# Kernel tuning notes

Hardware: AMD Instinct MI355X
Metric: run time of the kernel (lower is better)

Reference implementation:

```python
import jax, jax.numpy as jnp
import numpy as np

N_HEADS = 32
N_KV = 8
HEAD_DIM = 128
EPS = 1e-5

def _rope(t, fr, fi):
    # t: [b,s,h,hd] -> pairs [b,s,h,hd/2,2]; fr/fi: [s,hd/2]
    tp = t.astype(jnp.float32).reshape(*t.shape[:-1], HEAD_DIM // 2, 2)
    a, b = tp[..., 0], tp[..., 1]
    fr = fr[None, :, None, :]
    fi = fi[None, :, None, :]
    out = jnp.stack([a * fr - b * fi, a * fi + b * fr], axis=-1)
    return out.reshape(t.shape).astype(t.dtype)

def _rmsnorm(t):
    tf = t.astype(jnp.float32)
    return (tf * jax.lax.rsqrt(jnp.mean(tf * tf, axis=-1, keepdims=True) + EPS)).astype(t.dtype)

def setup_inputs() -> dict:
    key = jax.random.key(0)
    ks = jax.random.split(key, 5)
    b, s, dim = 1, 2048, 4096
    x = jax.random.normal(ks[0], (b, s, dim), dtype=jnp.float32) * 0.02
    wq = jax.random.normal(ks[1], (dim, dim), dtype=jnp.float32) * 0.02
    wk = jax.random.normal(ks[2], (N_KV * HEAD_DIM, dim), dtype=jnp.float32) * 0.02
    wv = jax.random.normal(ks[3], (N_KV * HEAD_DIM, dim), dtype=jnp.float32) * 0.02
    wo = jax.random.normal(ks[4], (dim, dim), dtype=jnp.float32) * 0.02
    # RoPE freqs, llama-style theta=10000
    inv = 1.0 / (10000.0 ** (np.arange(0, HEAD_DIM, 2, dtype=np.float32) / HEAD_DIM))
    ang = np.outer(np.arange(s, dtype=np.float32), inv)  # [s, hd/2]
    freqs_cis = jnp.asarray(np.stack([np.cos(ang), np.sin(ang)], axis=-1))  # [s, hd/2, 2]
    # causal additive mask
    mask = jnp.where(jnp.tril(jnp.ones((s, s), dtype=bool)), 0.0, -1e30).astype(jnp.float32)
    return {"x": x, "wq": wq, "wk": wk, "wv": wv, "wo": wo,
            "freqs_cis": freqs_cis, "mask": mask, "start_pos": 0}

def reference(x, wq, wk, wv, wo, freqs_cis, mask, start_pos):
    b, s, dim = x.shape
    n_rep = N_HEADS // N_KV
    xq = jnp.einsum('bsd,ed->bse', x, wq).reshape(b, s, N_HEADS, HEAD_DIM)
    xk = jnp.einsum('bsd,ed->bse', x, wk).reshape(b, s, N_KV, HEAD_DIM)
    xv = jnp.einsum('bsd,ed->bse', x, wv).reshape(b, s, N_KV, HEAD_DIM)
    fr, fi = freqs_cis[..., 0], freqs_cis[..., 1]
    xq = _rope(xq, fr, fi)
    xk = _rope(xk, fr, fi)
    xq = _rmsnorm(xq)
    xk = _rmsnorm(xk)
    # start_pos=0 prefill: KV cache write/read is identity on xk/xv
    q = xq.transpose(0, 2, 1, 3).reshape(b, N_KV, n_rep, s, HEAD_DIM)  # grouped query heads
    k = xk.transpose(0, 2, 1, 3)  # [b, n_kv, s, hd]
    v = xv.transpose(0, 2, 1, 3)
    scores = jnp.einsum('bkrsd,bktd->bkrst', q, k) / np.sqrt(HEAD_DIM)
    scores = scores + mask[None, None, None, :, :]
    probs = jax.nn.softmax(scores, axis=-1)
    o = jnp.einsum('bkrst,bktd->bkrsd', probs, v)
    o = o.reshape(b, N_HEADS, s, HEAD_DIM).transpose(0, 2, 1, 3).reshape(b, s, dim)
    return jnp.einsum('bse,de->bsd', o, wo)
```

## Files before the change

### kernel.cpp

```cpp
#include <hip/hip_runtime.h>
#include <hip/hip_bf16.h>
#include <cstdint>
#include <cstddef>

using u16 = unsigned short;
using u32 = unsigned int;

typedef __attribute__((ext_vector_type(8))) __bf16 bf16x8;
typedef __attribute__((ext_vector_type(4))) float f32x4;
typedef __attribute__((ext_vector_type(2))) float f32x2;
typedef __attribute__((ext_vector_type(4))) u32 u32x4;

typedef const __attribute__((address_space(1))) void* gas_ptr;
typedef __attribute__((address_space(3))) void* las_ptr;

__device__ __forceinline__ void async_cp16(const void* g, void* l) {
  __builtin_amdgcn_global_load_lds((gas_ptr)g, (las_ptr)l, 16, 0, 0);
}

__device__ __forceinline__ float bf2f(u16 u) {
  u32 v = ((u32)u) << 16;
  return __builtin_bit_cast(float, v);
}
__device__ __forceinline__ u16 f2bf(float f) {
  u32 v = __builtin_bit_cast(u32, f);
  u32 r = (v + 0x7fffu + ((v >> 16) & 1u)) >> 16;
  return (u16)r;
}

__device__ __forceinline__ f32x4 mfma16(bf16x8 a, bf16x8 b, f32x4 c) {
  return __builtin_amdgcn_mfma_f32_16x16x32_bf16(a, b, c, 0, 0, 0);
}

__global__ __launch_bounds__(256) void cvt_f32_bf16(const float* __restrict__ in,
                                                    u16* __restrict__ out, int n8) {
  int i = blockIdx.x * blockDim.x + threadIdx.x;
  int stride = gridDim.x * blockDim.x;
  for (; i < n8; i += stride) {
    const float4* p = (const float4*)(in + (size_t)i * 8);
    float4 a = p[0], b = p[1];
    union { u16 us[8]; u32x4 v; } o;
    o.us[0] = f2bf(a.x); o.us[1] = f2bf(a.y); o.us[2] = f2bf(a.z); o.us[3] = f2bf(a.w);
    o.us[4] = f2bf(b.x); o.us[5] = f2bf(b.y); o.us[6] = f2bf(b.z); o.us[7] = f2bf(b.w);
    *(u32x4*)(out + (size_t)i * 8) = o.v;
  }
}

template <bool F32OUT>
__global__ __launch_bounds__(256, 3) void gemm_bt(const u16* __restrict__ A,
                                                  const u16* __restrict__ B,
                                                  void* __restrict__ Cv,
                                                  int M, int N, int K) {
  __shared__ __align__(16) u16 As[128 * 64];
  __shared__ __align__(16) u16 Bs[128 * 64];
  const int tid = threadIdx.x;
  const int wave = tid >> 6, lane = tid & 63;
  const int quad = lane >> 4, c16 = lane & 15;

  const int mb = M >> 7, nb = N >> 7;
  const int per_xcd_n = nb >> 3;
  const int xcd = blockIdx.x & 7, lid = blockIdx.x >> 3;
  const int m_t = lid % mb, n_local = lid / mb;
  const int m0 = m_t * 128, n0 = (xcd * per_xcd_n + n_local) * 128;

  const int wm = (wave & 1) * 64, wn = (wave >> 1) * 64;

  f32x4 acc[4][4] = {};

  const u16* Ab = A + (size_t)m0 * K;
  const u16* Bb = B + (size_t)n0 * K;

  for (int k0 = 0; k0 < K; k0 += 64) {
    __syncthreads();
#pragma unroll
    for (int i = 0; i < 4; ++i) {
      int idx = tid + 256 * i;
      int row = idx >> 3, sg = (idx & 7) ^ (row & 7);
      async_cp16(Ab + (size_t)row * K + k0 + sg * 8, As + (size_t)idx * 8);
    }
#pragma unroll
    for (int i = 0; i < 4; ++i) {
      int idx = tid + 256 * i;
      int row = idx >> 3, sg = (idx & 7) ^ (row & 7);
      async_cp16(Bb + (size_t)row * K + k0 + sg * 8, Bs + (size_t)idx * 8);
    }
    asm volatile("s_waitcnt vmcnt(0)" ::: "memory");
    __syncthreads();

    bf16x8 af[4][2], bfr[4][2];
#pragma unroll
    for (int mt = 0; mt < 4; ++mt) {
      int row = wm + mt * 16 + c16;
#pragma unroll
      for (int c = 0; c < 2; ++c)
        af[mt][c] = *(const bf16x8*)(As + row * 64 + (((c * 4 + quad) ^ (row & 7)) * 8));
    }
#pragma unroll
    for (int nt = 0; nt < 4; ++nt) {
      int row = wn + nt * 16 + c16;
#pragma unroll
      for (int c = 0; c < 2; ++c)
        bfr[nt][c] = *(const bf16x8*)(Bs + row * 64 + (((c * 4 + quad) ^ (row & 7)) * 8));
    }
#pragma unroll
    for (int c = 0; c < 2; ++c)
#pragma unroll
      for (int mt = 0; mt < 4; ++mt)
#pragma unroll
        for (int nt = 0; nt < 4; ++nt)
          acc[mt][nt] = mfma16(af[mt][c], bfr[nt][c], acc[mt][nt]);
  }

#pragma unroll
  for (int mt = 0; mt < 4; ++mt) {
#pragma unroll
    for (int nt = 0; nt < 4; ++nt) {
#pragma unroll
      for (int r = 0; r < 4; ++r) {
        int gm = m0 + wm + mt * 16 + quad * 4 + r;
        int gn = n0 + wn + nt * 16 + c16;
        float v = acc[mt][nt][r];
        if (F32OUT)
          ((float*)Cv)[(size_t)gm * N + gn] = v;
        else
          ((u16*)Cv)[(size_t)gm * N + gn] = f2bf(v);
      }
    }
  }
}

__global__ __launch_bounds__(256) void transpose_v(const u16* __restrict__ in,
                                                   u16* __restrict__ out) {
  __shared__ __align__(16) u16 t[64 * 72];
  const int bs = blockIdx.x * 64;
  const int be = blockIdx.y * 64;
  const int tid = threadIdx.x;
  {
    const int row = tid >> 3, cc = tid & 7;
#pragma unroll
    for (int pp = 0; pp < 2; ++pp) {
      int r = row + 32 * pp;
      u32x4 v = *(const u32x4*)(in + (size_t)(bs + r) * 6144 + 5120 + be + cc * 8);
      *(u32x4*)(&t[r * 72 + ((cc ^ ((r >> 3) & 7)) * 8)]) = v;
    }
  }
  __syncthreads();
  {
    const int c0 = tid >> 3, rc = tid & 7;
#pragma unroll
    for (int pp = 0; pp < 2; ++pp) {
      int c = c0 + 32 * pp;
      union { u16 us[8]; u32x4 v; } o;
#pragma unroll
      for (int j = 0; j < 8; ++j)
        o.us[j] = t[(rc * 8 + j) * 72 + ((((c >> 3) ^ rc) * 8) + (c & 7))];
      *(u32x4*)(out + (size_t)(be + c) * 2048 + bs + rc * 8) = o.v;
    }
  }
}

__global__ __launch_bounds__(256) void rope_rms(const u16* __restrict__ in, int stride,
                                                u16* __restrict__ out,
                                                const float* __restrict__ freqs,
                                                int n_heads) {
  int gw = blockIdx.x * 4 + (threadIdx.x >> 6);
  int lane = threadIdx.x & 63;
  int s = gw / n_heads, h = gw % n_heads;
  u32 ab = *(const u32*)(in + (size_t)s * stride + h * 128 + lane * 2);
  float a = bf2f((u16)(ab & 0xffff));
  float b = bf2f((u16)(ab >> 16));
  f32x2 ff = *(const f32x2*)(freqs + (size_t)s * 128 + lane * 2);
  float ra = a * ff.x - b * ff.y;
  float rb = a * ff.y + b * ff.x;
  float ss = ra * ra + rb * rb;
#pragma unroll
  for (int m = 32; m; m >>= 1) ss += __shfl_xor(ss, m, 64);
  float r = rsqrtf(ss * (1.0f / 128.0f) + 1e-5f);
  u32 pk = (u32)f2bf(ra * r) | ((u32)f2bf(rb * r) << 16);
  *(u32*)(out + ((size_t)h * 2048 + s) * 128 + lane * 2) = pk;
}

#define SEQ 2048
__global__ __launch_bounds__(256) void attn(const u16* __restrict__ Q,
                                            const u16* __restrict__ Kh,
                                            const u16* __restrict__ VT,
                                            u16* __restrict__ O) {
  __shared__ __align__(16) u16 Ks[2][64 * 128];
  __shared__ __align__(16) u16 Vs[2][128 * 64];
  __shared__ __align__(16) u16 Ps[4][32 * 64];
  const int tid = threadIdx.x;
  const int wave = tid >> 6, lane = tid & 63;
  const int quad = lane >> 4, c16 = lane & 15;
  const int bid = blockIdx.x;
  const int hk = bid & 7;
  const int rest = bid >> 3;
  const int hq = rest >> 3;
  const int p = rest & 7;
  const int h = hk * 4 + hq;

  const float sc = 0.12751743f;
  const float B = 16.5f;
  const u16* Kb = Kh + (size_t)hk * SEQ * 128;
  const u16* Vb = VT + (size_t)hk * 128 * SEQ;

  auto stage = [&](int t0, int b) __attribute__((always_inline)) {
#pragma unroll
    for (int i = 0; i < 4; ++i) {
      int idx = tid + 256 * i;
      int row = idx >> 4, sg = (idx & 15) ^ (row & 7);
      async_cp16(Kb + (size_t)(t0 + row) * 128 + sg * 8, &Ks[b][(size_t)idx * 8]);
    }
#pragma unroll
    for (int i = 0; i < 4; ++i) {
      int idx = tid + 256 * i;
      int row = idx >> 3, sg = (idx & 7) ^ (row & 7);
      async_cp16(Vb + (size_t)row * SEQ + t0 + sg * 8, &Vs[b][(size_t)idx * 8]);
    }
  };

#pragma unroll 1
  for (int tile = 0; tile < 2; ++tile) {
    const int qt = tile ? (15 - p) : p;
    const int q0w = qt * 128 + wave * 32;
    const int kend = qt * 128 + 128;

    bf16x8 qfr[2][4];
    const u16* qbase = Q + (size_t)h * SEQ * 128;
#pragma unroll
    for (int g = 0; g < 2; ++g)
#pragma unroll
      for (int c = 0; c < 4; ++c)
        qfr[g][c] =
            *(const bf16x8*)(qbase + (size_t)(q0w + g * 16 + c16) * 128 + c * 32 + quad * 8);

    f32x4 o_acc[2][8] = {};
    float lsum[2][4] = {};

    __syncthreads();
    stage(0, 0);

#pragma unroll 1
    for (int t0 = 0; t0 < kend; t0 += 64) {
      const int cur = (t0 >> 6) & 1;
      asm volatile("s_waitcnt vmcnt(0)" ::: "memory");
      __syncthreads();
      if (t0 + 64 < kend) stage(t0 + 64, cur ^ 1);

      if (t0 < q0w + 32) {
        f32x4 sa[2][4] = {};
#pragma unroll
        for (int ct = 0; ct < 4; ++ct) {
          int t = ct * 16 + c16;
          int tbase = t * 128;
          int tsw = t & 7;
#pragma unroll
          for (int c = 0; c < 4; ++c) {
            bf16x8 kf = *(const bf16x8*)(&Ks[cur][tbase + (((c * 4 + quad) ^ tsw) * 8)]);
            sa[0][ct] = mfma16(qfr[0][c], kf, sa[0][ct]);
            sa[1][ct] = mfma16(qfr[1][c], kf, sa[1][ct]);
          }
        }

        const bool diag = (t0 + 64 > q0w);
        auto soft = [&](bool masked) __attribute__((always_inline)) {
#pragma unroll
          for (int g = 0; g < 2; ++g) {
#pragma unroll
            for (int r = 0; r < 4; ++r) {
              int row = g * 16 + quad * 4 + r;
              int row_q = q0w + row;
              int rbase = row * 64;
              int rsw = row & 7;
#pragma unroll
              for (int ct = 0; ct < 4; ++ct) {
                float s = sa[g][ct][r];
                float arg = fmaf(s, sc, -B);
                if (masked) {
                  int t_idx = t0 + ct * 16 + c16;
                  arg = (t_idx <= row_q) ? arg : -1.0e30f;
                }
                float pe = exp2f(arg);
                lsum[g][r] += pe;
                u32 pb = (__builtin_bit_cast(u32, pe) + 0x8000u) >> 16;
                Ps[wave][rbase + (((ct * 2 + (c16 >> 3)) ^ rsw) * 8) + (c16 & 7)] = (u16)pb;
              }
            }
          }
        };
        if (diag) soft(true); else soft(false);
        asm volatile("s_waitcnt lgkmcnt(0)" ::: "memory");

#pragma unroll
        for (int tc = 0; tc < 2; ++tc) {
          bf16x8 pf[2];
#pragma unroll
          for (int g = 0; g < 2; ++g) {
            int prow = g * 16 + c16;
            pf[g] = *(const bf16x8*)(&Ps[wave][prow * 64 + (((tc * 4 + quad) ^ (prow & 7)) * 8)]);
          }
#pragma unroll
          for (int nt = 0; nt < 8; ++nt) {
            int dl = nt * 16 + c16;
            bf16x8 vf = *(const bf16x8*)(&Vs[cur][dl * 64 + (((tc * 4 + quad) ^ (dl & 7)) * 8)]);
            o_acc[0][nt] = mfma16(pf[0], vf, o_acc[0][nt]);
            o_acc[1][nt] = mfma16(pf[1], vf, o_acc[1][nt]);
          }
        }
      }
    }

#pragma unroll
    for (int g = 0; g < 2; ++g) {
#pragma unroll
      for (int r = 0; r < 4; ++r) {
        float l = lsum[g][r];
#pragma unroll
        for (int m = 1; m < 16; m <<= 1) l += __shfl_xor(l, m, 64);
        float inv = 1.0f / l;
        int s_idx = q0w + g * 16 + quad * 4 + r;
        u16* ob = O + (size_t)s_idx * 4096 + (size_t)h * 128;
#pragma unroll
        for (int nt = 0; nt < 8; ++nt) ob[nt * 16 + c16] = f2bf(o_acc[g][nt][r] * inv);
      }
    }
  }
}

extern "C" void kernel_launch(void* const* d_in, const int* in_sizes, int n_in,
                              void* d_out, int out_size, void* d_ws, size_t ws_size,
                              hipStream_t stream) {
  const float* x  = (const float*)d_in[0];
  const float* wq = (const float*)d_in[1];
  const float* wk = (const float*)d_in[2];
  const float* wv = (const float*)d_in[3];
  const float* wo = (const float*)d_in[4];
  const float* fr = (const float*)d_in[5];
  float* out = (float*)d_out;

  const size_t S = 2048, D = 4096, KV = 1024, NQKV = D + 2 * KV;
  u16* p = (u16*)d_ws;
  u16* xb     = p; p += S * D;
  u16* wqkv   = p; p += NQKV * D;
  u16* qkvraw = p; p += S * NQKV;
  u16* qh     = p; p += S * D;
  u16* khh    = p; p += S * KV;
  u16* vt     = p; p += KV * S;
  u16* wob = wqkv;
  u16* ob  = qkvraw;

  auto cvt_launch = [&](const float* src, u16* dst, size_t n) {
    int n8 = (int)(n / 8);
    int blocks = (n8 + 255) / 256;
    if (blocks > 2048) blocks = 2048;
    cvt_f32_bf16<<<dim3(blocks), dim3(256), 0, stream>>>(src, dst, n8);
  };

  cvt_launch(x, xb, S * D);
  cvt_launch(wq, wqkv, D * D);
  cvt_launch(wk, wqkv + D * D, KV * D);
  cvt_launch(wv, wqkv + (D + KV) * D, KV * D);

  gemm_bt<false><<<dim3((S / 128) * (NQKV / 128)), dim3(256), 0, stream>>>(
      xb, wqkv, (void*)qkvraw, (int)S, (int)NQKV, (int)D);

  cvt_launch(wo, wob, D * D);

  transpose_v<<<dim3(32, 16), dim3(256), 0, stream>>>(qkvraw, vt);
  rope_rms<<<dim3((int)(S * 32 / 4)), dim3(256), 0, stream>>>(qkvraw, (int)NQKV, qh, fr, 32);
  rope_rms<<<dim3((int)(S * 8 / 4)), dim3(256), 0, stream>>>(qkvraw + D, (int)NQKV, khh, fr, 8);

  attn<<<dim3(256), dim3(256), 0, stream>>>(qh, khh, vt, ob);

  gemm_bt<true><<<dim3((S / 128) * (D / 128)), dim3(256), 0, stream>>>(
      ob, wob, (void*)out, (int)S, (int)D, (int)D);
}
```

Measured before the change: 483.3 us.

## Process paired causal query tiles concurrently in 512-thread attention blocks, fuse input conversions

The attention kernel now uses 512 threads per block. Two 4-wave groups handle the light and heavy query tiles of a causal pair at the same time, sharing one K/V staging pass, where before the two tiles ran one after the other. This avoids loading the light tile's K/V range twice and raises waves per CU; the block-to-head mapping changes and s_setprio hints are added around the MFMA loops. The four fp32-to-bf16 conversions of x, wq, wk and wv are merged into one launch to cut launch overhead. The risk is the light-tile group sitting idle at barriers while the heavy tile iterates, plus higher LDS use per block.

```diff
diff --git a/kernel.cpp b/kernel.cpp
--- a/kernel.cpp
+++ b/kernel.cpp
@@ -43,6 +43,33 @@
     o.us[0] = f2bf(a.x); o.us[1] = f2bf(a.y); o.us[2] = f2bf(a.z); o.us[3] = f2bf(a.w);
     o.us[4] = f2bf(b.x); o.us[5] = f2bf(b.y); o.us[6] = f2bf(b.z); o.us[7] = f2bf(b.w);
     *(u32x4*)(out + (size_t)i * 8) = o.v;
+  }
+}
+
+__global__ __launch_bounds__(256) void cvt4(const float* __restrict__ x,
+                                            const float* __restrict__ wq,
+                                            const float* __restrict__ wk,
+                                            const float* __restrict__ wv,
+                                            u16* __restrict__ xb,
+                                            u16* __restrict__ wqkv) {
+  const int B0 = 1048576;
+  const int B1 = B0 + 2097152;
+  const int B2 = B1 + 524288;
+  const int B3 = B2 + 524288;
+  int i = blockIdx.x * blockDim.x + threadIdx.x;
+  int stride = gridDim.x * blockDim.x;
+  for (; i < B3; i += stride) {
+    const float* src; u16* dst; int j;
+    if (i < B0)      { src = x;  dst = xb;                           j = i; }
+    else if (i < B1) { src = wq; dst = wqkv;                         j = i - B0; }
+    else if (i < B2) { src = wk; dst = wqkv + (size_t)4096 * 4096;   j = i - B1; }
+    else             { src = wv; dst = wqkv + (size_t)5120 * 4096;   j = i - B2; }
+    const float4* p = (const float4*)(src + (size_t)j * 8);
+    float4 a = p[0], b = p[1];
+    union { u16 us[8]; u32x4 v; } o;
+    o.us[0] = f2bf(a.x); o.us[1] = f2bf(a.y); o.us[2] = f2bf(a.z); o.us[3] = f2bf(a.w);
+    o.us[4] = f2bf(b.x); o.us[5] = f2bf(b.y); o.us[6] = f2bf(b.z); o.us[7] = f2bf(b.w);
+    *(u32x4*)(dst + (size_t)j * 8) = o.v;
   }
 }
 
@@ -181,22 +208,27 @@
 }
 
 #define SEQ 2048
-__global__ __launch_bounds__(256) void attn(const u16* __restrict__ Q,
-                                            const u16* __restrict__ Kh,
-                                            const u16* __restrict__ VT,
-                                            u16* __restrict__ O) {
+__global__ __launch_bounds__(512, 2) void attn(const u16* __restrict__ Q,
+                                               const u16* __restrict__ Kh,
+                                               const u16* __restrict__ VT,
+                                               u16* __restrict__ O) {
   __shared__ __align__(16) u16 Ks[2][64 * 128];
   __shared__ __align__(16) u16 Vs[2][128 * 64];
-  __shared__ __align__(16) u16 Ps[4][32 * 64];
+  __shared__ __align__(16) u16 Ps[8][32 * 64];
   const int tid = threadIdx.x;
   const int wave = tid >> 6, lane = tid & 63;
   const int quad = lane >> 4, c16 = lane & 15;
   const int bid = blockIdx.x;
   const int hk = bid & 7;
   const int rest = bid >> 3;
-  const int hq = rest >> 3;
-  const int p = rest & 7;
+  const int hq = rest & 3;
+  const int p = rest >> 2;
   const int h = hk * 4 + hq;
+
+  const int wl = wave & 3, grp = wave >> 2;
+  const int qt = grp ? p : (15 - p);
+  const int q0w = qt * 128 + wl * 32;
+  const int kend = (15 - p) * 128 + 128;
 
   const float sc = 0.12751743f;
   const float B = 16.5f;
@@ -205,123 +237,119 @@
 
   auto stage = [&](int t0, int b) __attribute__((always_inline)) {
 #pragma unroll
-    for (int i = 0; i < 4; ++i) {
-      int idx = tid + 256 * i;
+    for (int i = 0; i < 2; ++i) {
+      int idx = tid + 512 * i;
       int row = idx >> 4, sg = (idx & 15) ^ (row & 7);
       async_cp16(Kb + (size_t)(t0 + row) * 128 + sg * 8, &Ks[b][(size_t)idx * 8]);
     }
 #pragma unroll
-    for (int i = 0; i < 4; ++i) {
-      int idx = tid + 256 * i;
+    for (int i = 0; i < 2; ++i) {
+      int idx = tid + 512 * i;
       int row = idx >> 3, sg = (idx & 7) ^ (row & 7);
       async_cp16(Vb + (size_t)row * SEQ + t0 + sg * 8, &Vs[b][(size_t)idx * 8]);
     }
   };
 
+  bf16x8 qfr[2][4];
+  const u16* qbase = Q + (size_t)h * SEQ * 128;
+#pragma unroll
+  for (int g = 0; g < 2; ++g)
+#pragma unroll
+    for (int c = 0; c < 4; ++c)
+      qfr[g][c] =
+          *(const bf16x8*)(qbase + (size_t)(q0w + g * 16 + c16) * 128 + c * 32 + quad * 8);
+
+  f32x4 o_acc[2][8] = {};
+  float lsum[2][4] = {};
+
+  stage(0, 0);
+
 #pragma unroll 1
-  for (int tile = 0; tile < 2; ++tile) {
-    const int qt = tile ? (15 - p) : p;
-    const int q0w = qt * 128 + wave * 32;
-    const int kend = qt * 128 + 128;
-
-    bf16x8 qfr[2][4];
-    const u16* qbase = Q + (size_t)h * SEQ * 128;
-#pragma unroll
-    for (int g = 0; g < 2; ++g)
-#pragma unroll
-      for (int c = 0; c < 4; ++c)
-        qfr[g][c] =
-            *(const bf16x8*)(qbase + (size_t)(q0w + g * 16 + c16) * 128 + c * 32 + quad * 8);
-
-    f32x4 o_acc[2][8] = {};
-    float lsum[2][4] = {};
-
+  for (int t0 = 0; t0 < kend; t0 += 64) {
+    const int cur = (t0 >> 6) & 1;
+    asm volatile("s_waitcnt vmcnt(0)" ::: "memory");
     __syncthreads();
-    stage(0, 0);
-
-#pragma unroll 1
-    for (int t0 = 0; t0 < kend; t0 += 64) {
-      const int cur = (t0 >> 6) & 1;
-      asm volatile("s_waitcnt vmcnt(0)" ::: "memory");
-      __syncthreads();
-      if (t0 + 64 < kend) stage(t0 + 64, cur ^ 1);
-
-      if (t0 < q0w + 32) {
-        f32x4 sa[2][4] = {};
-#pragma unroll
-        for (int ct = 0; ct < 4; ++ct) {
-          int t = ct * 16 + c16;
-          int tbase = t * 128;
-          int tsw = t & 7;
-#pragma unroll
-          for (int c = 0; c < 4; ++c) {
-            bf16x8 kf = *(const bf16x8*)(&Ks[cur][tbase + (((c * 4 + quad) ^ tsw) * 8)]);
-            sa[0][ct] = mfma16(qfr[0][c], kf, sa[0][ct]);
-            sa[1][ct] = mfma16(qfr[1][c], kf, sa[1][ct]);
+    if (t0 + 64 < kend) stage(t0 + 64, cur ^ 1);
+
+    if (t0 < q0w + 32) {
+      f32x4 sa[2][4] = {};
+      __builtin_amdgcn_s_setprio(1);
+#pragma unroll
+      for (int ct = 0; ct < 4; ++ct) {
+        int t = ct * 16 + c16;
+        int tbase = t * 128;
+        int tsw = t & 7;
+#pragma unroll
+        for (int c = 0; c < 4; ++c) {
+          bf16x8 kf = *(const bf16x8*)(&Ks[cur][tbase + (((c * 4 + quad) ^ tsw) * 8)]);
+          sa[0][ct] = mfma16(qfr[0][c], kf, sa[0][ct]);
+          sa[1][ct] = mfma16(qfr[1][c], kf, sa[1][ct]);
+        }
+      }
+      __builtin_amdgcn_s_setprio(0);
+
+      const bool diag = (t0 + 64 > q0w);
+      auto soft = [&](bool masked) __attribute__((always_inline)) {
+#pragma unroll
+        for (int g = 0; g < 2; ++g) {
+#pragma unroll
+          for (int r = 0; r < 4; ++r) {
+            int row = g * 16 + quad * 4 + r;
+            int row_q = q0w + row;
+            int rbase = row * 64;
+            int rsw = row & 7;
+#pragma unroll
+            for (int ct = 0; ct < 4; ++ct) {
+              float s = sa[g][ct][r];
+              float arg = fmaf(s, sc, -B);
+              if (masked) {
+                int t_idx = t0 + ct * 16 + c16;
+                arg = (t_idx <= row_q) ? arg : -1.0e30f;
+              }
+              float pe = exp2f(arg);
+              lsum[g][r] += pe;
+              u32 pb = (__builtin_bit_cast(u32, pe) + 0x8000u) >> 16;
+              Ps[wave][rbase + (((ct * 2 + (c16 >> 3)) ^ rsw) * 8) + (c16 & 7)] = (u16)pb;
+            }
           }
         }
-
-        const bool diag = (t0 + 64 > q0w);
-        auto soft = [&](bool masked) __attribute__((always_inline)) {
-#pragma unroll
-          for (int g = 0; g < 2; ++g) {
-#pragma unroll
-            for (int r = 0; r < 4; ++r) {
-              int row = g * 16 + quad * 4 + r;
-              int row_q = q0w + row;
-              int rbase = row * 64;
-              int rsw = row & 7;
-#pragma unroll
-              for (int ct = 0; ct < 4; ++ct) {
-                float s = sa[g][ct][r];
-                float arg = fmaf(s, sc, -B);
-                if (masked) {
-                  int t_idx = t0 + ct * 16 + c16;
-                  arg = (t_idx <= row_q) ? arg : -1.0e30f;
-                }
-                float pe = exp2f(arg);
-                lsum[g][r] += pe;
-                u32 pb = (__builtin_bit_cast(u32, pe) + 0x8000u) >> 16;
-                Ps[wave][rbase + (((ct * 2 + (c16 >> 3)) ^ rsw) * 8) + (c16 & 7)] = (u16)pb;
-              }
-            }
-          }
-        };
-        if (diag) soft(true); else soft(false);
-        asm volatile("s_waitcnt lgkmcnt(0)" ::: "memory");
-
-#pragma unroll
-        for (int tc = 0; tc < 2; ++tc) {
-          bf16x8 pf[2];
-#pragma unroll
-          for (int g = 0; g < 2; ++g) {
-            int prow = g * 16 + c16;
-            pf[g] = *(const bf16x8*)(&Ps[wave][prow * 64 + (((tc * 4 + quad) ^ (prow & 7)) * 8)]);
-          }
-#pragma unroll
-          for (int nt = 0; nt < 8; ++nt) {
-            int dl = nt * 16 + c16;
-            bf16x8 vf = *(const bf16x8*)(&Vs[cur][dl * 64 + (((tc * 4 + quad) ^ (dl & 7)) * 8)]);
-            o_acc[0][nt] = mfma16(pf[0], vf, o_acc[0][nt]);
-            o_acc[1][nt] = mfma16(pf[1], vf, o_acc[1][nt]);
-          }
+      };
+      if (diag) soft(true); else soft(false);
+      asm volatile("s_waitcnt lgkmcnt(0)" ::: "memory");
+
+      __builtin_amdgcn_s_setprio(1);
+#pragma unroll
+      for (int tc = 0; tc < 2; ++tc) {
+        bf16x8 pf[2];
+#pragma unroll
+        for (int g = 0; g < 2; ++g) {
+          int prow = g * 16 + c16;
+          pf[g] = *(const bf16x8*)(&Ps[wave][prow * 64 + (((tc * 4 + quad) ^ (prow & 7)) * 8)]);
+        }
+#pragma unroll
+        for (int nt = 0; nt < 8; ++nt) {
+          int dl = nt * 16 + c16;
+          bf16x8 vf = *(const bf16x8*)(&Vs[cur][dl * 64 + (((tc * 4 + quad) ^ (dl & 7)) * 8)]);
+          o_acc[0][nt] = mfma16(pf[0], vf, o_acc[0][nt]);
+          o_acc[1][nt] = mfma16(pf[1], vf, o_acc[1][nt]);
         }
       }
-    }
-
-#pragma unroll
-    for (int g = 0; g < 2; ++g) {
-#pragma unroll
-      for (int r = 0; r < 4; ++r) {
-        float l = lsum[g][r];
-#pragma unroll
-        for (int m = 1; m < 16; m <<= 1) l += __shfl_xor(l, m, 64);
-        float inv = 1.0f / l;
-        int s_idx = q0w + g * 16 + quad * 4 + r;
-        u16* ob = O + (size_t)s_idx * 4096 + (size_t)h * 128;
-#pragma unroll
-        for (int nt = 0; nt < 8; ++nt) ob[nt * 16 + c16] = f2bf(o_acc[g][nt][r] * inv);
-      }
+      __builtin_amdgcn_s_setprio(0);
+    }
+  }
+
+#pragma unroll
+  for (int g = 0; g < 2; ++g) {
+#pragma unroll
+    for (int r = 0; r < 4; ++r) {
+      float l = lsum[g][r];
+#pragma unroll
+      for (int m = 1; m < 16; m <<= 1) l += __shfl_xor(l, m, 64);
+      float inv = 1.0f / l;
+      int s_idx = q0w + g * 16 + quad * 4 + r;
+      u16* ob = O + (size_t)s_idx * 4096 + (size_t)h * 128;
+#pragma unroll
+      for (int nt = 0; nt < 8; ++nt) ob[nt * 16 + c16] = f2bf(o_acc[g][nt][r] * inv);
     }
   }
 }
@@ -348,28 +376,21 @@
   u16* wob = wqkv;
   u16* ob  = qkvraw;
 
-  auto cvt_launch = [&](const float* src, u16* dst, size_t n) {
-    int n8 = (int)(n / 8);
-    int blocks = (n8 + 255) / 256;
-    if (blocks > 2048) blocks = 2048;
-    cvt_f32_bf16<<<dim3(blocks), dim3(256), 0, stream>>>(src, dst, n8);
-  };
-
-  cvt_launch(x, xb, S * D);
-  cvt_launch(wq, wqkv, D * D);
-  cvt_launch(wk, wqkv + D * D, KV * D);
-  cvt_launch(wv, wqkv + (D + KV) * D, KV * D);
+  cvt4<<<dim3(2048), dim3(256), 0, stream>>>(x, wq, wk, wv, xb, wqkv);
 
   gemm_bt<false><<<dim3((S / 128) * (NQKV / 128)), dim3(256), 0, stream>>>(
       xb, wqkv, (void*)qkvraw, (int)S, (int)NQKV, (int)D);
 
-  cvt_launch(wo, wob, D * D);
+  {
+    int n8 = (int)(D * D / 8);
+    cvt_f32_bf16<<<dim3(2048), dim3(256), 0, stream>>>(wo, wob, n8);
+  }
 
   transpose_v<<<dim3(32, 16), dim3(256), 0, stream>>>(qkvraw, vt);
   rope_rms<<<dim3((int)(S * 32 / 4)), dim3(256), 0, stream>>>(qkvraw, (int)NQKV, qh, fr, 32);
   rope_rms<<<dim3((int)(S * 8 / 4)), dim3(256), 0, stream>>>(qkvraw + D, (int)NQKV, khh, fr, 8);
 
-  attn<<<dim3(256), dim3(256), 0, stream>>>(qh, khh, vt, ob);
+  attn<<<dim3(256), dim3(512), 0, stream>>>(qh, khh, vt, ob);
 
   gemm_bt<true><<<dim3((S / 128) * (D / 128)), dim3(256), 0, stream>>>(
       ob, wob, (void*)out, (int)S, (int)D, (int)D);
```

New measurement: 487.6 us. No clear change (+0.9%).
